# Optimization experiments

Measured on AMD Instinct MI355X. Metric: run time of the kernel, lower is better.

## Reference

```python
import jax, jax.numpy as jnp
import numpy as np

ALPHA = 1.5      # entmax alpha (q parameter)
N_ITER = 50      # entmax-bisect iterations (entmax library default)
B, S, DM, H, HKV, HD = 1, 2048, 2048, 16, 4, 128
ROPE_THETA = 10000.0


def _entmax_p(x):
    """alpha-entmax along last axis via bisection on tau (matches entmax.EntmaxBisect)."""
    am1 = ALPHA - 1.0
    pw = 1.0 / am1
    X = x * am1
    d = x.shape[-1]
    max_val = jnp.max(X, axis=-1, keepdims=True)
    tau_lo = max_val - 1.0                      # _gp(1, alpha) = 1
    tau_hi = max_val - (1.0 / d) ** am1          # _gp(1/d, alpha)
    dm0 = tau_hi - tau_lo

    def body(i, carry):
        tau_lo, dm, tau_m = carry
        dm = dm * 0.5
        tau_m = tau_lo + dm
        p = jnp.maximum(X - tau_m, 0.0) ** pw
        f = jnp.sum(p, axis=-1, keepdims=True) - 1.0
        tau_lo = jnp.where(f >= 0, tau_m, tau_lo)
        return (tau_lo, dm, tau_m)

    tau_lo, dm, tau_m = jax.lax.fori_loop(0, N_ITER, body, (tau_lo, dm0, tau_lo))
    p = jnp.maximum(X - tau_m, 0.0) ** pw
    return p / jnp.sum(p, axis=-1, keepdims=True)  # ensure_sum_one


@jax.custom_vjp
def entmax_bisect(x):
    return _entmax_p(x)

def _emx_fwd(x):
    p = _entmax_p(x)
    return p, p

def _emx_bwd(p, g):
    # entmax library backward: gppr = p^(2-alpha) on support
    gppr = jnp.where(p > 0, p ** (2.0 - ALPHA), 0.0)
    dX = g * gppr
    q = jnp.sum(dX, axis=-1, keepdims=True) / jnp.sum(gppr, axis=-1, keepdims=True)
    return ((dX - q * gppr),)

entmax_bisect.defvjp(_emx_fwd, _emx_bwd)


def _rotate_half(x):
    x1, x2 = x[..., : HD // 2], x[..., HD // 2:]
    return jnp.concatenate([-x2, x1], axis=-1)


def setup_inputs() -> dict:
    key = jax.random.key(0)
    k1, k2, k3, k4, k5 = jax.random.split(key, 5)
    hidden_states = jax.random.normal(k1, (B, S, DM), dtype=jnp.float32)
    wq = jax.random.normal(k2, (H * HD, DM), dtype=jnp.float32) * 0.02
    wk = jax.random.normal(k3, (HKV * HD, DM), dtype=jnp.float32) * 0.02
    wv = jax.random.normal(k4, (HKV * HD, DM), dtype=jnp.float32) * 0.02
    wo = jax.random.normal(k5, (DM, H * HD), dtype=jnp.float32) * 0.02
    # real Llama RoPE position embeddings
    inv_freq = 1.0 / (ROPE_THETA ** (np.arange(0, HD, 2, dtype=np.float32) / HD))
    pos = np.arange(S, dtype=np.float32)
    freqs = pos[:, None] * inv_freq[None, :]          # [S, HD/2]
    emb = np.concatenate([freqs, freqs], axis=-1)     # [S, HD]
    cos = jnp.asarray(np.cos(emb))[None]              # [1, S, HD]
    sin = jnp.asarray(np.sin(emb))[None]
    return {"hidden_states": hidden_states, "cos": cos, "sin": sin,
            "wq": wq, "wk": wk, "wv": wv, "wo": wo}


def reference(hidden_states, cos, sin, wq, wk, wv, wo):
    b, s, _ = hidden_states.shape
    scaling = HD ** -0.5
    # QKV projections -> [B, H, S, HD]
    q = (hidden_states @ wq.T).reshape(b, s, H, HD).transpose(0, 2, 1, 3)
    k = (hidden_states @ wk.T).reshape(b, s, HKV, HD).transpose(0, 2, 1, 3)
    v = (hidden_states @ wv.T).reshape(b, s, HKV, HD).transpose(0, 2, 1, 3)
    # RoPE (cos/sin broadcast over head axis)
    c, sn = cos[:, None, :, :], sin[:, None, :, :]
    q = q * c + _rotate_half(q) * sn
    k = k * c + _rotate_half(k) * sn
    # GQA: repeat kv heads
    g = H // HKV
    k = jnp.repeat(k, g, axis=1)
    v = jnp.repeat(v, g, axis=1)
    scores = jnp.einsum('bhqd,bhkd->bhqk', q, k) * scaling
    causal = jnp.tril(jnp.ones((s, s), dtype=bool))
    scores = jnp.where(causal, scores, -jnp.inf)
    attn = entmax_bisect(scores)                      # [B, H, S, S]
    out = jnp.einsum('bhqk,bhkd->bhqd', attn, v)
    out = out.transpose(0, 2, 1, 3).reshape(b, s, H * HD)
    out = out @ wo.T
    return (out, attn)
```

## Files before the change

### kernel.cpp

```cpp
#include <hip/hip_runtime.h>

typedef __bf16 bf16;
typedef __bf16 bf16x4 __attribute__((ext_vector_type(4)));
typedef __bf16 bf16x8 __attribute__((ext_vector_type(8)));
typedef float f32x4 __attribute__((ext_vector_type(4)));
typedef float f32x2 __attribute__((ext_vector_type(2)));

#define S 2048
#define DM 2048
#define HD 128
#define H 16
#define NQKV 3072
#define AS_ITERS 3
#define NW_ITERS 4
#define BROW 556

__device__ __forceinline__ void gl2lds16(const void* g, void* l) {
    __builtin_amdgcn_global_load_lds(
        (const __attribute__((address_space(1))) void*)g,
        (__attribute__((address_space(3))) void*)l, 16, 0, 0);
}

__device__ __forceinline__ void nt_store4(f32x4 v, float* p) {
    __builtin_nontemporal_store(v, (f32x4*)p);
}

template <int CTRL, int RM>
__device__ __forceinline__ float dpp_zero(float x) {
    return __builtin_bit_cast(float, __builtin_amdgcn_update_dpp(
        0, __builtin_bit_cast(int, x), CTRL, RM, 0xf, false));
}
template <int CTRL, int RM>
__device__ __forceinline__ float dpp_self(float x) {
    int xi = __builtin_bit_cast(int, x);
    return __builtin_bit_cast(float, __builtin_amdgcn_update_dpp(xi, xi, CTRL, RM, 0xf, false));
}
__device__ __forceinline__ float wave_bcast63(float x) {
    return __builtin_bit_cast(float, __builtin_amdgcn_readlane(__builtin_bit_cast(int, x), 63));
}
__device__ __forceinline__ float wave_sum(float x) {
    x += dpp_zero<0x111, 0xf>(x);
    x += dpp_zero<0x112, 0xf>(x);
    x += dpp_zero<0x114, 0xf>(x);
    x += dpp_zero<0x118, 0xf>(x);
    x += dpp_zero<0x142, 0xa>(x);
    x += dpp_zero<0x143, 0xc>(x);
    return wave_bcast63(x);
}
__device__ __forceinline__ float wave_fmax(float x) {
    x = fmaxf(x, dpp_self<0x111, 0xf>(x));
    x = fmaxf(x, dpp_self<0x112, 0xf>(x));
    x = fmaxf(x, dpp_self<0x114, 0xf>(x));
    x = fmaxf(x, dpp_self<0x118, 0xf>(x));
    x = fmaxf(x, dpp_self<0x142, 0xa>(x));
    x = fmaxf(x, dpp_self<0x143, 0xc>(x));
    return wave_bcast63(x);
}

__global__ void cvt_all(const float* __restrict__ hid, const float* __restrict__ wq,
                        const float* __restrict__ wk, const float* __restrict__ wv,
                        const float* __restrict__ wo, bf16* __restrict__ bh,
                        bf16* __restrict__ bqkv, bf16* __restrict__ bwo) {
    int i = blockIdx.x * blockDim.x + threadIdx.x;
    const float* src;
    bf16* dst;
    int off;
    if (i < 1048576) { src = hid; dst = bh; off = i; }
    else if (i < 2097152) { src = wq; dst = bqkv; off = i - 1048576; }
    else if (i < 2359296) { src = wk; dst = bqkv + 2048 * 2048; off = i - 2097152; }
    else if (i < 2621440) { src = wv; dst = bqkv + 2048 * 2048 + 512 * 2048; off = i - 2359296; }
    else { src = wo; dst = bwo; off = i - 2621440; }
    float4 f = ((const float4*)src)[off];
    bf16x4 o;
    o[0] = (bf16)f.x; o[1] = (bf16)f.y; o[2] = (bf16)f.z; o[3] = (bf16)f.w;
    ((bf16x4*)dst)[off] = o;
}

__global__ __launch_bounds__(256) void gemm128_bt(const bf16* __restrict__ A,
                                                  const bf16* __restrict__ B,
                                                  float* __restrict__ C, int Ndim, int K) {
    __shared__ bf16 As[2][128 * 32];
    __shared__ bf16 Bs[2][128 * 32];
    int m0 = blockIdx.x * 128, n0 = blockIdx.y * 128;
    int t = threadIdx.x;
    int l = t & 63, w = t >> 6;
    int lane16 = l & 15, quad = l >> 4;

    int c0 = (w * 2) * 64 + l;
    int c1 = c0 + 64;
    const bf16* Abase = A + (size_t)m0 * K;
    const bf16* Bbase = B + (size_t)n0 * K;

    int wm = (w & 1) * 64, wn = (w >> 1) * 64;
    f32x4 acc[4][4];
#pragma unroll
    for (int i = 0; i < 4; i++)
#pragma unroll
        for (int j = 0; j < 4; j++) acc[i][j] = (f32x4){0.f, 0.f, 0.f, 0.f};

    auto stage = [&](int sel, int k0) {
        gl2lds16(Abase + (size_t)(c0 >> 2) * K + k0 + (c0 & 3) * 8, &As[sel][(w * 2) * 512]);
        gl2lds16(Abase + (size_t)(c1 >> 2) * K + k0 + (c1 & 3) * 8, &As[sel][(w * 2 + 1) * 512]);
        gl2lds16(Bbase + (size_t)(c0 >> 2) * K + k0 + (c0 & 3) * 8, &Bs[sel][(w * 2) * 512]);
        gl2lds16(Bbase + (size_t)(c1 >> 2) * K + k0 + (c1 & 3) * 8, &Bs[sel][(w * 2 + 1) * 512]);
    };

    stage(0, 0);
    __syncthreads();
    int cur = 0;
    for (int k0 = 0; k0 < K; k0 += 32) {
        if (k0 + 32 < K) stage(cur ^ 1, k0 + 32);
        bf16x8 af[4], bfr[4];
#pragma unroll
        for (int i = 0; i < 4; i++)
            af[i] = *(const bf16x8*)&As[cur][(wm + i * 16 + lane16) * 32 + quad * 8];
#pragma unroll
        for (int j = 0; j < 4; j++)
            bfr[j] = *(const bf16x8*)&Bs[cur][(wn + j * 16 + lane16) * 32 + quad * 8];
#pragma unroll
        for (int i = 0; i < 4; i++)
#pragma unroll
            for (int j = 0; j < 4; j++)
                acc[i][j] = __builtin_amdgcn_mfma_f32_16x16x32_bf16(af[i], bfr[j], acc[i][j], 0, 0, 0);
        __syncthreads();
        cur ^= 1;
    }
#pragma unroll
    for (int i = 0; i < 4; i++)
#pragma unroll
        for (int j = 0; j < 4; j++) {
            float* cp = C + (size_t)(m0 + wm + i * 16 + quad * 4) * Ndim + n0 + wn + j * 16 + lane16;
#pragma unroll
            for (int r = 0; r < 4; r++) cp[(size_t)r * Ndim] = acc[i][j][r];
        }
}

__global__ void rope_qk(const float* __restrict__ qkv, const float* __restrict__ cosb,
                        const float* __restrict__ sinb, bf16* __restrict__ qs,
                        bf16* __restrict__ kb) {
    int col = blockIdx.x * 256 + threadIdx.x;
    int s = blockIdx.y;
    const float* row = qkv + (size_t)s * NQKV;
    float v = row[col];
    if (col < DM) {
        int h = col >> 7, d = col & 127;
        float c = cosb[s * HD + d], sn = sinb[s * HD + d];
        float other = row[(h << 7) + ((d < 64) ? (d + 64) : (d - 64))];
        float rot = (d < 64) ? -other : other;
        float o = v * c + rot * sn;
        qs[((size_t)h * S + s) * HD + d] = (bf16)(o * 0.04419417382415922f);
    } else {
        int c2 = col - DM;
        int kv = c2 >> 7, d = c2 & 127;
        float c = cosb[s * HD + d], sn = sinb[s * HD + d];
        float other = row[DM + (kv << 7) + ((d < 64) ? (d + 64) : (d - 64))];
        float rot = (d < 64) ? -other : other;
        float o = v * c + rot * sn;
        kb[((size_t)kv * S + s) * HD + d] = (bf16)o;
    }
}

__global__ __launch_bounds__(256) void vtrans(const float* __restrict__ qkv, bf16* __restrict__ vT) {
    __shared__ bf16 tile[64][66];
    int s0 = blockIdx.x * 64, y0 = blockIdx.y * 64;
    int t = threadIdx.x;
    int ty = t & 63, tr = t >> 6;
#pragma unroll
    for (int i = 0; i < 16; i++) {
        int s = tr + i * 4;
        float v = qkv[(size_t)(s0 + s) * NQKV + 2560 + y0 + ty];
        tile[s][ty] = (bf16)v;
    }
    __syncthreads();
#pragma unroll
    for (int i = 0; i < 16; i++) {
        int y = tr + i * 4;
        vT[(size_t)(y0 + y) * S + s0 + ty] = tile[ty][y];
    }
}

template <int SEGS>
__device__ __forceinline__ void attn_body(const bf16* __restrict__ qs, const bf16* __restrict__ kb,
                                          const bf16* __restrict__ vT, float* __restrict__ attn,
                                          bf16* __restrict__ o, int r0, int h,
                                          float (&buf)[16][BROW]) {
    constexpr int NREG2 = SEGS * 4;
    int jlen = r0 + 16;
    int l = threadIdx.x & 63;
    int w = threadIdx.x >> 6;
    int lane16 = l & 15, quad = l >> 4;

    const bf16* qrow = qs + ((size_t)h * S + (r0 + lane16)) * HD + quad * 8;
    bf16x8 afrag[4];
#pragma unroll
    for (int kc = 0; kc < 4; kc++) afrag[kc] = *(const bf16x8*)(qrow + kc * 32);

    const bf16* kbase = kb + (size_t)(h >> 2) * S * HD;
    const bf16* vbase = vT + (size_t)(h >> 2) * HD * S;
    f32x2 xr[NREG2];

#pragma unroll
    for (int sgi = 0; sgi < SEGS; sgi++) {
        int j0 = sgi * 512;
#pragma unroll
        for (int tt = 0; tt < 2; tt++) {
            int t = w + tt * 16;
            int jt = j0 + t * 16;
            if (jt < jlen) {
                f32x4 acc = {0.f, 0.f, 0.f, 0.f};
                const bf16* kp = kbase + (size_t)(jt + lane16) * HD + quad * 8;
#pragma unroll
                for (int kc = 0; kc < 4; kc++) {
                    bf16x8 b = *(const bf16x8*)(kp + kc * 32);
                    acc = __builtin_amdgcn_mfma_f32_16x16x32_bf16(afrag[kc], b, acc, 0, 0, 0);
                }
                if (jt + 15 > r0) {
                    int jj = jt + lane16;
#pragma unroll
                    for (int r = 0; r < 4; r++) {
                        int rowi = quad * 4 + r;
                        float v = acc[r];
                        if (jj > r0 + rowi) v = -1e30f;
                        buf[rowi][t * 16 + lane16] = v;
                    }
                } else {
#pragma unroll
                    for (int r = 0; r < 4; r++) buf[quad * 4 + r][t * 16 + lane16] = acc[r];
                }
            }
        }
        __syncthreads();
#pragma unroll
        for (int part = 0; part < 2; part++) {
            float4 fq = *(const float4*)&buf[w][part * 256 + l * 4];
            if (sgi == SEGS - 1) {
                int jb = j0 + part * 256 + l * 4;
                xr[sgi * 4 + part * 2 + 0] =
                    (f32x2){(jb + 0 < jlen) ? fq.x : -1e30f, (jb + 1 < jlen) ? fq.y : -1e30f};
                xr[sgi * 4 + part * 2 + 1] =
                    (f32x2){(jb + 2 < jlen) ? fq.z : -1e30f, (jb + 3 < jlen) ? fq.w : -1e30f};
            } else {
                xr[sgi * 4 + part * 2 + 0] = (f32x2){fq.x, fq.y};
                xr[sgi * 4 + part * 2 + 1] = (f32x2){fq.z, fq.w};
            }
        }
        __syncthreads();
    }

    float* arow = attn + ((size_t)h * S + (r0 + w)) * S;

    {
        f32x4 z4 = {0.f, 0.f, 0.f, 0.f};
        for (int j = SEGS * 512 + l * 4; j < S; j += 256) nt_store4(z4, &arow[j]);
    }

    const f32x2 z2 = {0.f, 0.f};
    float mx = -1e30f;
#pragma unroll
    for (int c = 0; c < NREG2; c++) mx = fmaxf(mx, fmaxf(xr[c][0], xr[c][1]));
    float m = wave_fmax(mx);
    float taulo = m - 1.0f;
    float tauhi = m - 0.02209709f;
    float tau = taulo;

#pragma unroll 1
    for (int it = 0; it < AS_ITERS; it++) {
        f32x2 tvi = {tau, tau};
        f32x2 b1a = z2, b1b = z2, b2a = z2, b2b = z2, cna = z2, cnb = z2;
#pragma unroll
        for (int c = 0; c < NREG2; c += 2) {
            f32x2 t0 = __builtin_elementwise_max(xr[c] - tvi, z2);
            b2a += t0 * t0; b1a += t0;
            cna += (f32x2){t0[0] > 0.f ? 1.f : 0.f, t0[1] > 0.f ? 1.f : 0.f};
            f32x2 t1 = __builtin_elementwise_max(xr[c + 1] - tvi, z2);
            b2b += t1 * t1; b1b += t1;
            cnb += (f32x2){t1[0] > 0.f ? 1.f : 0.f, t1[1] > 0.f ? 1.f : 0.f};
        }
        f32x2 s1 = b1a + b1b, s2 = b2a + b2b, sc = cna + cnb;
        float B1 = wave_sum(s1[0] + s1[1]);
        float B2 = wave_sum(s2[0] + s2[1]);
        float n = wave_sum(sc[0] + sc[1]);
        float disc = fmaxf(B1 * B1 - n * (B2 - 1.0f), 0.f);
        tau += (B1 - __builtin_sqrtf(disc)) / fmaxf(n, 1.0f);
        tau = fminf(fmaxf(tau, taulo), tauhi);
    }
#pragma unroll 1
    for (int it = 0; it < NW_ITERS; it++) {
        f32x2 tvi = {tau, tau};
        f32x2 fa = z2, fb = z2, ga = z2, gb = z2;
#pragma unroll
        for (int c = 0; c < NREG2; c += 2) {
            f32x2 t0 = __builtin_elementwise_max(xr[c] - tvi, z2);
            fa += t0 * t0; ga += t0;
            f32x2 t1 = __builtin_elementwise_max(xr[c + 1] - tvi, z2);
            fb += t1 * t1; gb += t1;
        }
        f32x2 fv = fa + fb, gv = ga + gb;
        float f = wave_sum(fv[0] + fv[1]);
        float g = wave_sum(gv[0] + gv[1]);
        tau += (f - 1.0f) / (2.0f * g + 1e-20f);
        tau = fminf(fmaxf(tau, taulo), tauhi);
    }

    f32x2 tv = {tau, tau};
    float inv;
    {
        f32x2 sa = z2, sbv = z2;
#pragma unroll
        for (int c = 0; c < NREG2; c += 2) {
            f32x2 t0 = __builtin_elementwise_max(xr[c] - tv, z2);
            sa += t0 * t0;
            f32x2 t1 = __builtin_elementwise_max(xr[c + 1] - tv, z2);
            sbv += t1 * t1;
        }
        f32x2 sv = sa + sbv;
        float ssum = wave_sum(sv[0] + sv[1]);
        inv = 1.0f / ssum;
    }

    int jt_o = (w & 7) * 16;
    int kh = (w >> 3) * 256;
    f32x4 acc_o = {0.f, 0.f, 0.f, 0.f};
    f32x2 inv2 = {inv, inv};

#pragma unroll
    for (int sgi = 0; sgi < SEGS; sgi++) {
        int j0 = sgi * 512;
        bf16 (*pb)[BROW] = (bf16(*)[BROW])(&buf[0][0]) + (sgi & 1) * 16;
#pragma unroll
        for (int part = 0; part < 2; part++) {
            f32x2 ta = __builtin_elementwise_max(xr[sgi * 4 + part * 2 + 0] - tv, z2);
            f32x2 tb = __builtin_elementwise_max(xr[sgi * 4 + part * 2 + 1] - tv, z2);
            f32x2 pa = (ta * ta) * inv2;
            f32x2 pb2 = (tb * tb) * inv2;
            f32x4 pv = {pa[0], pa[1], pb2[0], pb2[1]};
            nt_store4(pv, &arow[j0 + part * 256 + l * 4]);
            bf16x4 pbv;
            pbv[0] = (bf16)pv[0]; pbv[1] = (bf16)pv[1];
            pbv[2] = (bf16)pv[2]; pbv[3] = (bf16)pv[3];
            *(bf16x4*)&pb[w][part * 256 + l * 4] = pbv;
        }
        __syncthreads();
#pragma unroll
        for (int ks = 0; ks < 8; ks++) {
            int kk = kh + ks * 32;
            bf16x8 a = *(const bf16x8*)&pb[lane16][kk + quad * 8];
            bf16x8 b = *(const bf16x8*)(vbase + (size_t)(jt_o + lane16) * S + j0 + kk + quad * 8);
            acc_o = __builtin_amdgcn_mfma_f32_16x16x32_bf16(a, b, acc_o, 0, 0, 0);
        }
    }

    __syncthreads();
    if (w >= 8) {
#pragma unroll
        for (int r = 0; r < 4; r++) buf[w - 8][l * 4 + r] = acc_o[r];
    }
    __syncthreads();
    if (w < 8) {
        bf16* op = o + (size_t)(r0 + quad * 4) * DM + h * HD + jt_o + lane16;
#pragma unroll
        for (int r = 0; r < 4; r++) {
            float v = acc_o[r] + buf[w][l * 4 + r];
            op[(size_t)r * DM] = (bf16)v;
        }
    }
}

__global__ __launch_bounds__(1024, 8) void attn_av_all(const bf16* __restrict__ qs,
                                                       const bf16* __restrict__ kb,
                                                       const bf16* __restrict__ vT,
                                                       float* __restrict__ attn,
                                                       bf16* __restrict__ o) {
    __shared__ float buf[16][BROW];
    int b = blockIdx.x;
    int h = b & 15;
    int qh = b >> 4;
    attn_body<4>(qs, kb, vT, attn, o, (96 + qh) * 16, h, buf);
    __syncthreads();
    attn_body<3>(qs, kb, vT, attn, o, (64 + qh) * 16, h, buf);
    __syncthreads();
    attn_body<2>(qs, kb, vT, attn, o, (32 + qh) * 16, h, buf);
    __syncthreads();
    attn_body<1>(qs, kb, vT, attn, o, qh * 16, h, buf);
}

extern "C" void kernel_launch(void* const* d_in, const int* in_sizes, int n_in,
                              void* d_out, int out_size, void* d_ws, size_t ws_size,
                              hipStream_t stream) {
    const float* hidden = (const float*)d_in[0];
    const float* cosb   = (const float*)d_in[1];
    const float* sinb   = (const float*)d_in[2];
    const float* wq     = (const float*)d_in[3];
    const float* wk     = (const float*)d_in[4];
    const float* wv     = (const float*)d_in[5];
    const float* wo     = (const float*)d_in[6];
    char* ws = (char*)d_ws;
    bf16*  bf_hidden = (bf16*)(ws);
    bf16*  bf_wqkv   = (bf16*)(ws + 8388608);
    bf16*  bf_wo     = (bf16*)(ws + 20971520);
    float* qkv_raw   = (float*)(ws + 29360128);
    bf16*  qsb       = (bf16*)(ws + 54525952);
    bf16*  kbb       = (bf16*)(ws + 62914560);
    bf16*  vTb       = (bf16*)(ws + 65011712);
    float* out  = (float*)d_out;
    float* attn = out + 4194304;

    cvt_all<<<dim3(14336), 256, 0, stream>>>(hidden, wq, wk, wv, wo, bf_hidden, bf_wqkv, bf_wo);

    gemm128_bt<<<dim3(16, 24), 256, 0, stream>>>(bf_hidden, bf_wqkv, qkv_raw, NQKV, DM);

    rope_qk<<<dim3(10, S), 256, 0, stream>>>(qkv_raw, cosb, sinb, qsb, kbb);
    vtrans<<<dim3(32, 8), 256, 0, stream>>>(qkv_raw, vTb);

    attn_av_all<<<dim3(512), 1024, 0, stream>>>(qsb, kbb, vTb, attn, bf_hidden);

    gemm128_bt<<<dim3(16, 16), 256, 0, stream>>>(bf_hidden, bf_wo, out, DM, DM);
}
```

Before: 586.8 us.

## Fuse RoPE and V transpose into QKV GEMM epilogue, retile output GEMM

The QKV projection GEMM now applies RoPE, scales Q, and writes bf16 Q/K plus the transposed V directly through a shared-memory staging tile. This removes the fp32 qkv intermediate buffer and the separate rope and transpose kernels. Both GEMMs switch to 64x128 tiles, doubling the block count to improve occupancy. The entmax Newton iteration count is also reduced from 4 to 3, which trims attention work but risks a less converged threshold.

```diff
diff --git a/kernel.cpp b/kernel.cpp
--- a/kernel.cpp
+++ b/kernel.cpp
@@ -12,7 +12,7 @@
 #define H 16
 #define NQKV 3072
 #define AS_ITERS 3
-#define NW_ITERS 4
+#define NW_ITERS 3
 #define BROW 556
 
 __device__ __forceinline__ void gl2lds16(const void* g, void* l) {
@@ -76,33 +76,49 @@
     ((bf16x4*)dst)[off] = o;
 }
 
-__global__ __launch_bounds__(256) void gemm128_bt(const bf16* __restrict__ A,
-                                                  const bf16* __restrict__ B,
-                                                  float* __restrict__ C, int Ndim, int K) {
-    __shared__ bf16 As[2][128 * 32];
-    __shared__ bf16 Bs[2][128 * 32];
-    int m0 = blockIdx.x * 128, n0 = blockIdx.y * 128;
+__global__ __launch_bounds__(256) void gemm_qkv_rope(const bf16* __restrict__ A,
+                                                     const bf16* __restrict__ B,
+                                                     const float* __restrict__ cosb,
+                                                     const float* __restrict__ sinb,
+                                                     bf16* __restrict__ qs,
+                                                     bf16* __restrict__ kb,
+                                                     bf16* __restrict__ vT) {
+    constexpr int BM = 64, BN = 128, K = DM;
+    __shared__ bf16 As[2][BM * 32];
+    __shared__ bf16 Bs[2][BN * 32];
+    __shared__ float ct[32][129];
+    int m0 = blockIdx.x * BM;
+    int by = blockIdx.y;
+    int n0 = by * BN;
     int t = threadIdx.x;
     int l = t & 63, w = t >> 6;
     int lane16 = l & 15, quad = l >> 4;
 
-    int c0 = (w * 2) * 64 + l;
-    int c1 = c0 + 64;
     const bf16* Abase = A + (size_t)m0 * K;
     const bf16* Bbase = B + (size_t)n0 * K;
 
-    int wm = (w & 1) * 64, wn = (w >> 1) * 64;
-    f32x4 acc[4][4];
-#pragma unroll
-    for (int i = 0; i < 4; i++)
-#pragma unroll
-        for (int j = 0; j < 4; j++) acc[i][j] = (f32x4){0.f, 0.f, 0.f, 0.f};
+    constexpr int MI = BM / 32, NI = BN / 32;
+    int wm = (w & 1) * (BM / 2), wn = (w >> 1) * (BN / 2);
+    f32x4 acc[MI][NI];
+#pragma unroll
+    for (int i = 0; i < MI; i++)
+#pragma unroll
+        for (int j = 0; j < NI; j++) acc[i][j] = (f32x4){0.f, 0.f, 0.f, 0.f};
+
+    constexpr int AG = BM * 4;
+    constexpr int BG = BN * 4;
 
     auto stage = [&](int sel, int k0) {
-        gl2lds16(Abase + (size_t)(c0 >> 2) * K + k0 + (c0 & 3) * 8, &As[sel][(w * 2) * 512]);
-        gl2lds16(Abase + (size_t)(c1 >> 2) * K + k0 + (c1 & 3) * 8, &As[sel][(w * 2 + 1) * 512]);
-        gl2lds16(Bbase + (size_t)(c0 >> 2) * K + k0 + (c0 & 3) * 8, &Bs[sel][(w * 2) * 512]);
-        gl2lds16(Bbase + (size_t)(c1 >> 2) * K + k0 + (c1 & 3) * 8, &Bs[sel][(w * 2 + 1) * 512]);
+#pragma unroll
+        for (int it = 0; it < AG / 256; it++) {
+            int c = it * 256 + t;
+            gl2lds16(Abase + (size_t)(c >> 2) * K + k0 + (c & 3) * 8, &As[sel][(c - l) * 8]);
+        }
+#pragma unroll
+        for (int it = 0; it < BG / 256; it++) {
+            int c = it * 256 + t;
+            gl2lds16(Bbase + (size_t)(c >> 2) * K + k0 + (c & 3) * 8, &Bs[sel][(c - l) * 8]);
+        }
     };
 
     stage(0, 0);
@@ -110,73 +126,129 @@
     int cur = 0;
     for (int k0 = 0; k0 < K; k0 += 32) {
         if (k0 + 32 < K) stage(cur ^ 1, k0 + 32);
-        bf16x8 af[4], bfr[4];
-#pragma unroll
-        for (int i = 0; i < 4; i++)
+        bf16x8 af[MI], bfr[NI];
+#pragma unroll
+        for (int i = 0; i < MI; i++)
             af[i] = *(const bf16x8*)&As[cur][(wm + i * 16 + lane16) * 32 + quad * 8];
 #pragma unroll
-        for (int j = 0; j < 4; j++)
+        for (int j = 0; j < NI; j++)
             bfr[j] = *(const bf16x8*)&Bs[cur][(wn + j * 16 + lane16) * 32 + quad * 8];
 #pragma unroll
-        for (int i = 0; i < 4; i++)
-#pragma unroll
-            for (int j = 0; j < 4; j++)
+        for (int i = 0; i < MI; i++)
+#pragma unroll
+            for (int j = 0; j < NI; j++)
                 acc[i][j] = __builtin_amdgcn_mfma_f32_16x16x32_bf16(af[i], bfr[j], acc[i][j], 0, 0, 0);
         __syncthreads();
         cur ^= 1;
     }
-#pragma unroll
-    for (int i = 0; i < 4; i++)
-#pragma unroll
-        for (int j = 0; j < 4; j++) {
+
+#pragma unroll
+    for (int half = 0; half < 2; half++) {
+        if ((w & 1) == half) {
+#pragma unroll
+            for (int i = 0; i < MI; i++)
+#pragma unroll
+                for (int j = 0; j < NI; j++)
+#pragma unroll
+                    for (int r = 0; r < 4; r++)
+                        ct[i * 16 + quad * 4 + r][wn + j * 16 + lane16] = acc[i][j][r];
+        }
+        __syncthreads();
+        if (by < 20) {
+#pragma unroll
+            for (int it = 0; it < 16; it++) {
+                int idx = it * 256 + t;
+                int row = idx >> 7, d = idx & 127;
+                int s = m0 + half * 32 + row;
+                float v = ct[row][d];
+                float other = ct[row][(d < 64) ? (d + 64) : (d - 64)];
+                float c = cosb[s * HD + d], sn = sinb[s * HD + d];
+                float rot = (d < 64) ? -other : other;
+                float o = v * c + rot * sn;
+                if (by < 16)
+                    qs[((size_t)by * S + s) * HD + d] = (bf16)(o * 0.04419417382415922f);
+                else
+                    kb[((size_t)(by - 16) * S + s) * HD + d] = (bf16)o;
+            }
+        } else {
+            int y0 = (by - 20) * 128;
+#pragma unroll
+            for (int it = 0; it < 16; it++) {
+                int idx = it * 256 + t;
+                int y = idx >> 5, ss = idx & 31;
+                vT[(size_t)(y0 + y) * S + m0 + half * 32 + ss] = (bf16)ct[ss][y];
+            }
+        }
+        __syncthreads();
+    }
+}
+
+template <int BM, int BN>
+__global__ __launch_bounds__(256) void gemm_bt(const bf16* __restrict__ A,
+                                               const bf16* __restrict__ B,
+                                               float* __restrict__ C, int Ndim, int K) {
+    __shared__ bf16 As[2][BM * 32];
+    __shared__ bf16 Bs[2][BN * 32];
+    int m0 = blockIdx.x * BM, n0 = blockIdx.y * BN;
+    int t = threadIdx.x;
+    int l = t & 63, w = t >> 6;
+    int lane16 = l & 15, quad = l >> 4;
+
+    const bf16* Abase = A + (size_t)m0 * K;
+    const bf16* Bbase = B + (size_t)n0 * K;
+
+    constexpr int MI = BM / 32, NI = BN / 32;
+    int wm = (w & 1) * (BM / 2), wn = (w >> 1) * (BN / 2);
+    f32x4 acc[MI][NI];
+#pragma unroll
+    for (int i = 0; i < MI; i++)
+#pragma unroll
+        for (int j = 0; j < NI; j++) acc[i][j] = (f32x4){0.f, 0.f, 0.f, 0.f};
+
+    constexpr int AG = BM * 4;
+    constexpr int BG = BN * 4;
+
+    auto stage = [&](int sel, int k0) {
+#pragma unroll
+        for (int it = 0; it < AG / 256; it++) {
+            int c = it * 256 + t;
+            gl2lds16(Abase + (size_t)(c >> 2) * K + k0 + (c & 3) * 8, &As[sel][(c - l) * 8]);
+        }
+#pragma unroll
+        for (int it = 0; it < BG / 256; it++) {
+            int c = it * 256 + t;
+            gl2lds16(Bbase + (size_t)(c >> 2) * K + k0 + (c & 3) * 8, &Bs[sel][(c - l) * 8]);
+        }
+    };
+
+    stage(0, 0);
+    __syncthreads();
+    int cur = 0;
+    for (int k0 = 0; k0 < K; k0 += 32) {
+        if (k0 + 32 < K) stage(cur ^ 1, k0 + 32);
+        bf16x8 af[MI], bfr[NI];
+#pragma unroll
+        for (int i = 0; i < MI; i++)
+            af[i] = *(const bf16x8*)&As[cur][(wm + i * 16 + lane16) * 32 + quad * 8];
+#pragma unroll
+        for (int j = 0; j < NI; j++)
+            bfr[j] = *(const bf16x8*)&Bs[cur][(wn + j * 16 + lane16) * 32 + quad * 8];
+#pragma unroll
+        for (int i = 0; i < MI; i++)
+#pragma unroll
+            for (int j = 0; j < NI; j++)
+                acc[i][j] = __builtin_amdgcn_mfma_f32_16x16x32_bf16(af[i], bfr[j], acc[i][j], 0, 0, 0);
+        __syncthreads();
+        cur ^= 1;
+    }
+#pragma unroll
+    for (int i = 0; i < MI; i++)
+#pragma unroll
+        for (int j = 0; j < NI; j++) {
             float* cp = C + (size_t)(m0 + wm + i * 16 + quad * 4) * Ndim + n0 + wn + j * 16 + lane16;
 #pragma unroll
             for (int r = 0; r < 4; r++) cp[(size_t)r * Ndim] = acc[i][j][r];
         }
-}
-
-__global__ void rope_qk(const float* __restrict__ qkv, const float* __restrict__ cosb,
-                        const float* __restrict__ sinb, bf16* __restrict__ qs,
-                        bf16* __restrict__ kb) {
-    int col = blockIdx.x * 256 + threadIdx.x;
-    int s = blockIdx.y;
-    const float* row = qkv + (size_t)s * NQKV;
-    float v = row[col];
-    if (col < DM) {
-        int h = col >> 7, d = col & 127;
-        float c = cosb[s * HD + d], sn = sinb[s * HD + d];
-        float other = row[(h << 7) + ((d < 64) ? (d + 64) : (d - 64))];
-        float rot = (d < 64) ? -other : other;
-        float o = v * c + rot * sn;
-        qs[((size_t)h * S + s) * HD + d] = (bf16)(o * 0.04419417382415922f);
-    } else {
-        int c2 = col - DM;
-        int kv = c2 >> 7, d = c2 & 127;
-        float c = cosb[s * HD + d], sn = sinb[s * HD + d];
-        float other = row[DM + (kv << 7) + ((d < 64) ? (d + 64) : (d - 64))];
-        float rot = (d < 64) ? -other : other;
-        float o = v * c + rot * sn;
-        kb[((size_t)kv * S + s) * HD + d] = (bf16)o;
-    }
-}
-
-__global__ __launch_bounds__(256) void vtrans(const float* __restrict__ qkv, bf16* __restrict__ vT) {
-    __shared__ bf16 tile[64][66];
-    int s0 = blockIdx.x * 64, y0 = blockIdx.y * 64;
-    int t = threadIdx.x;
-    int ty = t & 63, tr = t >> 6;
-#pragma unroll
-    for (int i = 0; i < 16; i++) {
-        int s = tr + i * 4;
-        float v = qkv[(size_t)(s0 + s) * NQKV + 2560 + y0 + ty];
-        tile[s][ty] = (bf16)v;
-    }
-    __syncthreads();
-#pragma unroll
-    for (int i = 0; i < 16; i++) {
-        int y = tr + i * 4;
-        vT[(size_t)(y0 + y) * S + s0 + ty] = tile[ty][y];
-    }
 }
 
 template <int SEGS>
@@ -398,21 +470,18 @@
     bf16*  bf_hidden = (bf16*)(ws);
     bf16*  bf_wqkv   = (bf16*)(ws + 8388608);
     bf16*  bf_wo     = (bf16*)(ws + 20971520);
-    float* qkv_raw   = (float*)(ws + 29360128);
-    bf16*  qsb       = (bf16*)(ws + 54525952);
-    bf16*  kbb       = (bf16*)(ws + 62914560);
-    bf16*  vTb       = (bf16*)(ws + 65011712);
+    bf16*  qsb       = (bf16*)(ws + 29360128);
+    bf16*  kbb       = (bf16*)(ws + 37748736);
+    bf16*  vTb       = (bf16*)(ws + 39845888);
     float* out  = (float*)d_out;
     float* attn = out + 4194304;
 
     cvt_all<<<dim3(14336), 256, 0, stream>>>(hidden, wq, wk, wv, wo, bf_hidden, bf_wqkv, bf_wo);
 
-    gemm128_bt<<<dim3(16, 24), 256, 0, stream>>>(bf_hidden, bf_wqkv, qkv_raw, NQKV, DM);
-
-    rope_qk<<<dim3(10, S), 256, 0, stream>>>(qkv_raw, cosb, sinb, qsb, kbb);
-    vtrans<<<dim3(32, 8), 256, 0, stream>>>(qkv_raw, vTb);
+    gemm_qkv_rope<<<dim3(32, 24), 256, 0, stream>>>(bf_hidden, bf_wqkv, cosb, sinb,
+                                                    qsb, kbb, vTb);
 
     attn_av_all<<<dim3(512), 1024, 0, stream>>>(qsb, kbb, vTb, attn, bf_hidden);
 
-    gemm128_bt<<<dim3(16, 16), 256, 0, stream>>>(bf_hidden, bf_wo, out, DM, DM);
-}
+    gemm_bt<64, 128><<<dim3(32, 16), 256, 0, stream>>>(bf_hidden, bf_wo, out, DM, DM);
+}
```

After: 567.1 us. 1.03x faster.

## Fuse RoPE and V transpose into QKV GEMM epilogue, cut Newton iterations

Applied to the files above, without the earlier changes.

Adds a QKV projection GEMM whose epilogue stages each 32-row slice of the output tile through LDS, then applies RoPE and the scaling for Q/K columns and writes V transposed, all in bf16. This removes the fp32 qkv intermediate buffer and two separate kernels (rope_qk, vtrans) along with their global traffic and launches. Separately, NW_ITERS is lowered from 4 to 3, cutting one Newton refinement step in the entmax threshold solve, which may reduce accuracy. The epilogue adds extra syncthreads per tile.

```diff
diff --git a/kernel.cpp b/kernel.cpp
--- a/kernel.cpp
+++ b/kernel.cpp
@@ -12,7 +12,7 @@
 #define H 16
 #define NQKV 3072
 #define AS_ITERS 3
-#define NW_ITERS 4
+#define NW_ITERS 3
 #define BROW 556
 
 __device__ __forceinline__ void gl2lds16(const void* g, void* l) {
@@ -76,6 +76,109 @@
     ((bf16x4*)dst)[off] = o;
 }
 
+__global__ __launch_bounds__(256) void gemm_qkv_rope(const bf16* __restrict__ A,
+                                                     const bf16* __restrict__ B,
+                                                     const float* __restrict__ cosb,
+                                                     const float* __restrict__ sinb,
+                                                     bf16* __restrict__ qs,
+                                                     bf16* __restrict__ kb,
+                                                     bf16* __restrict__ vT) {
+    constexpr int K = DM;
+    __shared__ bf16 smem[2][8192];
+    int m0 = blockIdx.x * 128;
+    int by = blockIdx.y;
+    int n0 = by * 128;
+    int t = threadIdx.x;
+    int l = t & 63, w = t >> 6;
+    int lane16 = l & 15, quad = l >> 4;
+
+    int c0 = (w * 2) * 64 + l;
+    int c1 = c0 + 64;
+    const bf16* Abase = A + (size_t)m0 * K;
+    const bf16* Bbase = B + (size_t)n0 * K;
+
+    int wm = (w & 1) * 64, wn = (w >> 1) * 64;
+    f32x4 acc[4][4];
+#pragma unroll
+    for (int i = 0; i < 4; i++)
+#pragma unroll
+        for (int j = 0; j < 4; j++) acc[i][j] = (f32x4){0.f, 0.f, 0.f, 0.f};
+
+    auto stage = [&](int sel, int k0) {
+        bf16* As = &smem[sel][0];
+        bf16* Bs = &smem[sel][4096];
+        gl2lds16(Abase + (size_t)(c0 >> 2) * K + k0 + (c0 & 3) * 8, &As[(w * 2) * 512]);
+        gl2lds16(Abase + (size_t)(c1 >> 2) * K + k0 + (c1 & 3) * 8, &As[(w * 2 + 1) * 512]);
+        gl2lds16(Bbase + (size_t)(c0 >> 2) * K + k0 + (c0 & 3) * 8, &Bs[(w * 2) * 512]);
+        gl2lds16(Bbase + (size_t)(c1 >> 2) * K + k0 + (c1 & 3) * 8, &Bs[(w * 2 + 1) * 512]);
+    };
+
+    stage(0, 0);
+    __syncthreads();
+    int cur = 0;
+    for (int k0 = 0; k0 < K; k0 += 32) {
+        if (k0 + 32 < K) stage(cur ^ 1, k0 + 32);
+        const bf16* As = &smem[cur][0];
+        const bf16* Bs = &smem[cur][4096];
+        bf16x8 af[4], bfr[4];
+#pragma unroll
+        for (int i = 0; i < 4; i++)
+            af[i] = *(const bf16x8*)&As[(wm + i * 16 + lane16) * 32 + quad * 8];
+#pragma unroll
+        for (int j = 0; j < 4; j++)
+            bfr[j] = *(const bf16x8*)&Bs[(wn + j * 16 + lane16) * 32 + quad * 8];
+#pragma unroll
+        for (int i = 0; i < 4; i++)
+#pragma unroll
+            for (int j = 0; j < 4; j++)
+                acc[i][j] = __builtin_amdgcn_mfma_f32_16x16x32_bf16(af[i], bfr[j], acc[i][j], 0, 0, 0);
+        __syncthreads();
+        cur ^= 1;
+    }
+
+    float (*ct)[129] = (float(*)[129]) & smem[0][0];
+#pragma unroll
+    for (int hf = 0; hf < 4; hf++) {
+        if ((w & 1) == (hf >> 1)) {
+            int ibase = (hf & 1) * 2;
+#pragma unroll
+            for (int ii = 0; ii < 2; ii++)
+#pragma unroll
+                for (int j = 0; j < 4; j++)
+#pragma unroll
+                    for (int r = 0; r < 4; r++)
+                        ct[ii * 16 + quad * 4 + r][wn + j * 16 + lane16] = acc[ibase + ii][j][r];
+        }
+        __syncthreads();
+        if (by < 20) {
+#pragma unroll
+            for (int it2 = 0; it2 < 16; it2++) {
+                int idx = it2 * 256 + t;
+                int row = idx >> 7, d = idx & 127;
+                int s = m0 + hf * 32 + row;
+                float v = ct[row][d];
+                float other = ct[row][(d < 64) ? (d + 64) : (d - 64)];
+                float c = cosb[s * HD + d], sn = sinb[s * HD + d];
+                float rot = (d < 64) ? -other : other;
+                float o = v * c + rot * sn;
+                if (by < 16)
+                    qs[((size_t)by * S + s) * HD + d] = (bf16)(o * 0.04419417382415922f);
+                else
+                    kb[((size_t)(by - 16) * S + s) * HD + d] = (bf16)o;
+            }
+        } else {
+            int y0 = (by - 20) * 128;
+#pragma unroll
+            for (int it2 = 0; it2 < 16; it2++) {
+                int idx = it2 * 256 + t;
+                int y = idx >> 5, ss = idx & 31;
+                vT[(size_t)(y0 + y) * S + m0 + hf * 32 + ss] = (bf16)ct[ss][y];
+            }
+        }
+        __syncthreads();
+    }
+}
+
 __global__ __launch_bounds__(256) void gemm128_bt(const bf16* __restrict__ A,
                                                   const bf16* __restrict__ B,
                                                   float* __restrict__ C, int Ndim, int K) {
@@ -133,50 +236,6 @@
 #pragma unroll
             for (int r = 0; r < 4; r++) cp[(size_t)r * Ndim] = acc[i][j][r];
         }
-}
-
-__global__ void rope_qk(const float* __restrict__ qkv, const float* __restrict__ cosb,
-                        const float* __restrict__ sinb, bf16* __restrict__ qs,
-                        bf16* __restrict__ kb) {
-    int col = blockIdx.x * 256 + threadIdx.x;
-    int s = blockIdx.y;
-    const float* row = qkv + (size_t)s * NQKV;
-    float v = row[col];
-    if (col < DM) {
-        int h = col >> 7, d = col & 127;
-        float c = cosb[s * HD + d], sn = sinb[s * HD + d];
-        float other = row[(h << 7) + ((d < 64) ? (d + 64) : (d - 64))];
-        float rot = (d < 64) ? -other : other;
-        float o = v * c + rot * sn;
-        qs[((size_t)h * S + s) * HD + d] = (bf16)(o * 0.04419417382415922f);
-    } else {
-        int c2 = col - DM;
-        int kv = c2 >> 7, d = c2 & 127;
-        float c = cosb[s * HD + d], sn = sinb[s * HD + d];
-        float other = row[DM + (kv << 7) + ((d < 64) ? (d + 64) : (d - 64))];
-        float rot = (d < 64) ? -other : other;
-        float o = v * c + rot * sn;
-        kb[((size_t)kv * S + s) * HD + d] = (bf16)o;
-    }
-}
-
-__global__ __launch_bounds__(256) void vtrans(const float* __restrict__ qkv, bf16* __restrict__ vT) {
-    __shared__ bf16 tile[64][66];
-    int s0 = blockIdx.x * 64, y0 = blockIdx.y * 64;
-    int t = threadIdx.x;
-    int ty = t & 63, tr = t >> 6;
-#pragma unroll
-    for (int i = 0; i < 16; i++) {
-        int s = tr + i * 4;
-        float v = qkv[(size_t)(s0 + s) * NQKV + 2560 + y0 + ty];
-        tile[s][ty] = (bf16)v;
-    }
-    __syncthreads();
-#pragma unroll
-    for (int i = 0; i < 16; i++) {
-        int y = tr + i * 4;
-        vT[(size_t)(y0 + y) * S + s0 + ty] = tile[ty][y];
-    }
 }
 
 template <int SEGS>
@@ -398,19 +457,16 @@
     bf16*  bf_hidden = (bf16*)(ws);
     bf16*  bf_wqkv   = (bf16*)(ws + 8388608);
     bf16*  bf_wo     = (bf16*)(ws + 20971520);
-    float* qkv_raw   = (float*)(ws + 29360128);
-    bf16*  qsb       = (bf16*)(ws + 54525952);
-    bf16*  kbb       = (bf16*)(ws + 62914560);
-    bf16*  vTb       = (bf16*)(ws + 65011712);
+    bf16*  qsb       = (bf16*)(ws + 29360128);
+    bf16*  kbb       = (bf16*)(ws + 37748736);
+    bf16*  vTb       = (bf16*)(ws + 39845888);
     float* out  = (float*)d_out;
     float* attn = out + 4194304;
 
     cvt_all<<<dim3(14336), 256, 0, stream>>>(hidden, wq, wk, wv, wo, bf_hidden, bf_wqkv, bf_wo);
 
-    gemm128_bt<<<dim3(16, 24), 256, 0, stream>>>(bf_hidden, bf_wqkv, qkv_raw, NQKV, DM);
-
-    rope_qk<<<dim3(10, S), 256, 0, stream>>>(qkv_raw, cosb, sinb, qsb, kbb);
-    vtrans<<<dim3(32, 8), 256, 0, stream>>>(qkv_raw, vTb);
+    gemm_qkv_rope<<<dim3(16, 24), 256, 0, stream>>>(bf_hidden, bf_wqkv, cosb, sinb,
+                                                    qsb, kbb, vTb);
 
     attn_av_all<<<dim3(512), 1024, 0, stream>>>(qsb, kbb, vTb, attn, bf_hidden);
 
```

Measured after the change: 564.4 us. -3.8%, faster.
